# Performance work log

Hardware: AMD Instinct MI355X
Metric: run time of the kernel (lower is better)

The kernel has to match this reference:

```python
import jax, jax.numpy as jnp
import numpy as np

NHEAD = 8

def layernorm(x, g, b, eps=1e-5):
    mu = x.mean(-1, keepdims=True)
    var = ((x - mu) ** 2).mean(-1, keepdims=True)
    return (x - mu) / jnp.sqrt(var + eps) * g + b

def linear_attention(q, k, v, eps=1e-6):
    # LoFTR kernelized linear attention: phi(x) = elu(x) + 1
    Q = jax.nn.elu(q) + 1.0          # [n, l, h, d]
    K = jax.nn.elu(k) + 1.0          # [n, s, h, d]
    s_len = v.shape[1]
    KV = jnp.einsum("nshd,nshv->nhdv", K, v / s_len)
    Z = 1.0 / (jnp.einsum("nlhd,nhd->nlh", Q, K.sum(axis=1)) + eps)
    return jnp.einsum("nlhd,nhdv,nlh->nlhv", Q, KV, Z) * s_len

def _block(x_base, q, k, v, Wm, W1, W2, g1, b1, g2, b2):
    bs, L, h, dh = q.shape
    msg = linear_attention(q, k, v).reshape(bs, L, h * dh)
    msg = layernorm(msg @ Wm, g1, b1)
    hcat = jnp.concatenate([x_base, msg], axis=2)          # [bs, L, 2*d]
    out = jax.nn.relu(hcat @ W1) @ W2
    return layernorm(out, g2, b2)

def setup_inputs() -> dict:
    key = jax.random.key(0)
    ks = jax.random.split(key, 8)
    bs, L, S, d = 8, 4800, 4800, 256
    w = lambda k, i, o: jax.random.normal(k, (i, o), jnp.float32) * 0.02
    return {
        "x": jax.random.normal(ks[0], (bs, L, d), jnp.float32),
        "source": jax.random.normal(ks[1], (bs, S, d), jnp.float32),
        "Wq": w(ks[2], d, d), "Wk": w(ks[3], d, d), "Wv": w(ks[4], d, d),
        "Wm": w(ks[5], d, d),
        "W1": w(ks[6], 2 * d, 2 * d), "W2": w(ks[7], 2 * d, d),
        "g1": jnp.ones((d,), jnp.float32), "b1": jnp.zeros((d,), jnp.float32),
        "g2": jnp.ones((d,), jnp.float32), "b2": jnp.zeros((d,), jnp.float32),
    }

def reference(x, source, Wq, Wk, Wv, Wm, W1, W2, g1, b1, g2, b2):
    bs, L, d = x.shape
    h = NHEAD
    dh = d // h
    q = (x @ Wq).reshape(bs, L, h, dh)
    k = (source @ Wk).reshape(bs, -1, h, dh)
    v = (source @ Wv).reshape(bs, -1, h, dh)
    # permute-then-view reinterpretations, exactly as in the torch code
    p13 = lambda t: t.transpose(0, 1, 3, 2).reshape(bs, -1, h, dh)  # permute(0,1,3,2)
    p21 = lambda t: t.transpose(0, 2, 1, 3).reshape(bs, -1, h, dh)  # permute(0,2,1,3)
    p32 = lambda t: t.transpose(0, 3, 2, 1).reshape(bs, -1, h, dh)  # permute(0,3,2,1)
    blk = lambda xb, qq, kk, vv: _block(xb, qq, kk, vv, Wm, W1, W2, g1, b1, g2, b2)
    m = blk(x, q, k, v)
    m3 = blk(x, p13(q), p13(k), p13(v))
    x_mid = x + 0.5 * (m + m3)
    m1 = blk(x_mid, p21(q), p21(k), p21(v))
    m2 = blk(x_mid, p32(q), p32(k), p32(v))
    return x_mid + 0.5 * (m1 + m2)
```

## Files before the change

### kernel.cpp

```cpp
#include <hip/hip_runtime.h>
#include <type_traits>
#include <cstdint>
#include <cstddef>

#define L_SEQ 4800
#define DMODEL 256
#define BS 8
#define MROWS (BS*L_SEQ)
#define PERBATCH (L_SEQ*DMODEL)
#define KVSET 67584

typedef __attribute__((ext_vector_type(8))) short bfrag8;
typedef __attribute__((ext_vector_type(4))) float floatx4;

__device__ __forceinline__ float bf2f(unsigned short u){
  union { unsigned int i; float f; } x; x.i = ((unsigned int)u) << 16; return x.f;
}
__device__ __forceinline__ unsigned short f2bf(float f){
  union { float f; unsigned int i; } x; x.f = f;
  x.i += 0x7fff + ((x.i >> 16) & 1);
  return (unsigned short)(x.i >> 16);
}
__device__ __forceinline__ float phi(float x){
  return x > 0.f ? x + 1.f : __expf(x);
}
__device__ __forceinline__ void gll16(const void* g, void* l){
  __builtin_amdgcn_global_load_lds((const __attribute__((address_space(1))) unsigned int*)g,
      (__attribute__((address_space(3))) unsigned int*)l, 16, 0, 0);
}

template<typename TC, bool RELU>
__global__ __launch_bounds__(256) void gemm_mfma(const unsigned short* __restrict__ A,
                                                 const unsigned short* __restrict__ Bt,
                                                 TC* __restrict__ C, int M, int N, int K){
  __shared__ unsigned short Al[2][4096];
  __shared__ unsigned short Bl[2][4096];
  const int tid  = threadIdx.x;
  const int lane = tid & 63;
  const int wave = tid >> 6;
  const int row0 = blockIdx.y << 7;
  const int col0 = blockIdx.x << 7;
  const int wr0  = (wave & 1) << 6;
  const int wc0  = (wave >> 1) << 6;
  const int m = lane & 15, q = lane >> 4;
  const int sw = (m >> 1) & 3;

  floatx4 acc[4][4] = {};

  const int u0 = tid, u1 = tid + 256;
  const int r0 = u0 >> 2, s0 = u0 & 3;
  const int r1 = u1 >> 2, s1 = u1 & 3;

  auto stage = [&](int k0, int b){
    gll16(A  + (size_t)(row0 + r0)*K + k0 + ((s0 ^ ((r0 >> 1) & 3)) << 3), Al[b] + (size_t)u0*8);
    gll16(A  + (size_t)(row0 + r1)*K + k0 + ((s1 ^ ((r1 >> 1) & 3)) << 3), Al[b] + (size_t)u1*8);
    gll16(Bt + (size_t)(col0 + r0)*K + k0 + ((s0 ^ ((r0 >> 1) & 3)) << 3), Bl[b] + (size_t)u0*8);
    gll16(Bt + (size_t)(col0 + r1)*K + k0 + ((s1 ^ ((r1 >> 1) & 3)) << 3), Bl[b] + (size_t)u1*8);
  };

  stage(0, 0);
  const int nk = K >> 5;
  for (int ks = 0; ks < nk; ks++){
    asm volatile("s_waitcnt vmcnt(0) lgkmcnt(0)" ::: "memory");
    __builtin_amdgcn_s_barrier();
    asm volatile("" ::: "memory");
    if (ks < nk - 1) stage((ks + 1) << 5, (ks + 1) & 1);
    const unsigned short* ab = Al[ks & 1];
    const unsigned short* bb = Bl[ks & 1];
    bfrag8 af[4], bf[4];
    #pragma unroll
    for (int t = 0; t < 4; t++){
      af[t] = *(const bfrag8*)(ab + (size_t)(wr0 + t*16 + m)*32 + ((q ^ sw) << 3));
      bf[t] = *(const bfrag8*)(bb + (size_t)(wc0 + t*16 + m)*32 + ((q ^ sw) << 3));
    }
    #pragma unroll
    for (int mt = 0; mt < 4; mt++)
      #pragma unroll
      for (int nt = 0; nt < 4; nt++)
        acc[mt][nt] = __builtin_amdgcn_mfma_f32_16x16x32_bf16(af[mt], bf[nt], acc[mt][nt], 0, 0, 0);
  }

  #pragma unroll
  for (int mt = 0; mt < 4; mt++){
    #pragma unroll
    for (int nt = 0; nt < 4; nt++){
      const int col  = col0 + wc0 + nt*16 + m;
      const int rowb = row0 + wr0 + mt*16 + q*4;
      #pragma unroll
      for (int i = 0; i < 4; i++){
        float v = acc[mt][nt][i];
        if (RELU) v = v > 0.f ? v : 0.f;
        if constexpr (std::is_same<TC,float>::value) C[(size_t)(rowb+i)*N + col] = v;
        else                                         C[(size_t)(rowb+i)*N + col] = f2bf(v);
      }
    }
  }
}

__global__ __launch_bounds__(256) void wconv(const float* __restrict__ W, unsigned short* __restrict__ Wt,
                                             int kshift, int N){
  int idx = blockIdx.x*256 + threadIdx.x;
  int kk = idx & ((1 << kshift) - 1);
  int nn = idx >> kshift;
  Wt[idx] = f2bf(W[(size_t)kk*N + nn]);
}
__global__ __launch_bounds__(256) void conv_bf16(const float* __restrict__ in, unsigned short* __restrict__ out){
  int i = blockIdx.x*256 + threadIdx.x;
  float4 v = ((const float4*)in)[i];
  ushort4 o; o.x = f2bf(v.x); o.y = f2bf(v.y); o.z = f2bf(v.z); o.w = f2bf(v.w);
  ((ushort4*)out)[i] = o;
}

__global__ __launch_bounds__(256) void permute1(const unsigned short* __restrict__ sA, unsigned short* __restrict__ dA,
                                                const unsigned short* __restrict__ sB, unsigned short* __restrict__ dB){
  const unsigned short* s = blockIdx.z ? sB : sA;
  unsigned short*       d = blockIdx.z ? dB : dA;
  __shared__ unsigned short tile[1024];
  const int t = threadIdx.x;
  const size_t base = (size_t)blockIdx.x * 1024;
  #pragma unroll
  for (int i = 0; i < 4; i++) tile[i*256 + t] = s[base + i*256 + t];
  __syncthreads();
  const int pg = ((t & 7) << 5) + (t >> 3);
  #pragma unroll
  for (int i = 0; i < 4; i++) d[base + i*256 + t] = tile[i*256 + pg];
}

__global__ __launch_bounds__(256) void permute2(const unsigned short* __restrict__ sA, unsigned short* __restrict__ dA,
                                                const unsigned short* __restrict__ sB, unsigned short* __restrict__ dB){
  const unsigned short* s = blockIdx.z ? sB : sA;
  unsigned short*       d = blockIdx.z ? dB : dA;
  __shared__ unsigned short tile[64*256];
  const int t = threadIdx.x;
  const int rr0 = blockIdx.x * 64;
  const size_t boff = (size_t)blockIdx.y * PERBATCH;
  #pragma unroll
  for (int i = 0; i < 16; i++){
    int u = i*256 + t;
    *(ushort4*)&tile[u*4] = *(const ushort4*)&s[boff + (size_t)rr0*256 + (size_t)u*4];
  }
  __syncthreads();
  #pragma unroll
  for (int i = 0; i < 8; i++){
    #pragma unroll
    for (int w = 0; w < 2; w++){
      int u = w*256 + t;
      int rr = u >> 3, c4 = (u & 7) << 2;
      ushort4 v = *(const ushort4*)&tile[rr*256 + i*32 + c4];
      *(ushort4*)&d[boff + (size_t)i*153600 + (size_t)rr0*32 + (size_t)u*4] = v;
    }
  }
}

__global__ __launch_bounds__(256) void permute3(const unsigned short* __restrict__ sA, unsigned short* __restrict__ dA,
                                                const unsigned short* __restrict__ sB, unsigned short* __restrict__ dB){
  const unsigned short* s = blockIdx.z ? sB : sA;
  unsigned short*       d = blockIdx.z ? dB : dA;
  __shared__ unsigned short tile[64*258];
  const int t = threadIdx.x;
  const int ll0 = blockIdx.x * 64;
  const size_t boff = (size_t)blockIdx.y * PERBATCH;
  #pragma unroll
  for (int i = 0; i < 32; i++){
    int u = i*256 + t;
    int row = u >> 7, col = (u & 127) << 1;
    *(ushort2*)&tile[row*258 + col] = *(const ushort2*)&s[boff + (size_t)(ll0+row)*256 + col];
  }
  __syncthreads();
  const int cw = t >> 6;
  const int ll = t & 63;
  #pragma unroll
  for (int cc = 0; cc < 256; cc += 4){
    int c = cc + cw;
    int sigma = ((c & 31) << 3) + (c >> 5);
    d[boff + (size_t)sigma*4800 + ll0 + ll] = tile[ll*258 + c];
  }
}

__global__ __launch_bounds__(256) void attn_stats(const unsigned short* __restrict__ kq,
                                                  const unsigned short* __restrict__ vq,
                                                  float* __restrict__ KV, float* __restrict__ Ksum){
  const int chunk = blockIdx.x, h = blockIdx.y, n = blockIdx.z;
  const int t = threadIdx.x;
  const int d = t >> 3;
  const int w4 = (t & 7) << 2;
  const size_t boff = (size_t)n * PERBATCH;
  __shared__ float kb[8][32], vb[8][32];
  const int lr = t >> 5, lj = t & 31;
  float a0=0.f, a1=0.f, a2=0.f, a3=0.f, ks=0.f;
  const int s0 = chunk * 240;
  for (int s = s0; s < s0 + 240; s += 8){
    int srci = (s + lr)*256 + (h << 5) + lj;
    kb[lr][lj] = phi(bf2f(kq[boff + srci]));
    vb[lr][lj] = bf2f(vq[boff + srci]);
    __syncthreads();
    #pragma unroll
    for (int r = 0; r < 8; r++){
      float kd = kb[r][d];
      ks += kd;
      a0 += kd * vb[r][w4+0];
      a1 += kd * vb[r][w4+1];
      a2 += kd * vb[r][w4+2];
      a3 += kd * vb[r][w4+3];
    }
    __syncthreads();
  }
  float* kvp = KV + (size_t)((((n<<3)+h)<<5) + d)*32 + w4;
  atomicAdd(kvp+0, a0);
  atomicAdd(kvp+1, a1);
  atomicAdd(kvp+2, a2);
  atomicAdd(kvp+3, a3);
  if ((t & 7) == 0) atomicAdd(Ksum + (((n<<3)+h)<<5) + d, ks);
}

__global__ __launch_bounds__(256) void attn_fused(const unsigned short* __restrict__ qq,
                                                  const float* __restrict__ KV,
                                                  const float* __restrict__ Ksum,
                                                  const unsigned short* __restrict__ WmT,
                                                  const float* __restrict__ g1,
                                                  const float* __restrict__ b1,
                                                  unsigned short* __restrict__ hcat){
  __shared__ float kvs[8192];
  __shared__ float Qs[4096];
  __shared__ float kss[256];
  __shared__ char  msgL[8192];
  __shared__ float2 LNp[16][4];
  const int t = threadIdx.x;
  const int n = blockIdx.y;
  const int row0 = blockIdx.x << 4;
  const size_t boff = (size_t)n * PERBATCH;

  {
    const float4* kvsrc = (const float4*)(KV + (size_t)n*8192);
    #pragma unroll
    for (int i = 0; i < 8; i++) ((float4*)kvs)[i*256 + t] = kvsrc[i*256 + t];
    kss[t] = Ksum[n*256 + t];
    #pragma unroll
    for (int i = 0; i < 4; i++){
      int u = (i << 8) + t;
      int r = u >> 6, c4 = (u & 63) << 2;
      ushort4 v = *(const ushort4*)(qq + boff + (size_t)(row0 + r)*256 + c4);
      float4 f;
      f.x = phi(bf2f(v.x)); f.y = phi(bf2f(v.y)); f.z = phi(bf2f(v.z)); f.w = phi(bf2f(v.w));
      *(float4*)&Qs[r*256 + c4] = f;
    }
  }
  __syncthreads();

  {
    const int h = t >> 5, w = t & 31;
    const float* kvh = kvs + h*1024;
    const float* ksh = kss + h*32;
    float acc[16], den[16];
    #pragma unroll
    for (int r = 0; r < 16; r++){ acc[r] = 0.f; den[r] = 1e-6f; }
    #pragma unroll
    for (int d4 = 0; d4 < 8; d4++){
      const float k0 = kvh[(d4*4+0)*32 + w];
      const float k1 = kvh[(d4*4+1)*32 + w];
      const float k2 = kvh[(d4*4+2)*32 + w];
      const float k3 = kvh[(d4*4+3)*32 + w];
      const float s0 = ksh[d4*4+0], s1 = ksh[d4*4+1], s2 = ksh[d4*4+2], s3 = ksh[d4*4+3];
      #pragma unroll
      for (int r = 0; r < 16; r++){
        float4 qv = *(const float4*)&Qs[r*256 + h*32 + d4*4];
        acc[r] += qv.x*k0 + qv.y*k1 + qv.z*k2 + qv.w*k3;
        den[r] += qv.x*s0 + qv.y*s1 + qv.z*s2 + qv.w*s3;
      }
    }
    #pragma unroll
    for (int r = 0; r < 16; r++){
      int byte = (r << 9) + ((t << 1) ^ ((r & 7) << 4));
      *(unsigned short*)(msgL + byte) = f2bf(acc[r] / den[r]);
    }
  }
  __syncthreads();

  const int wv = t >> 6, lane = t & 63, m = lane & 15, qd = lane >> 4;
  floatx4 Cf[4] = {};
  #pragma unroll
  for (int ks = 0; ks < 8; ks++){
    int abyte = m*512 + ((ks*64 + qd*16) ^ ((m & 7) << 4));
    bfrag8 af = *(const bfrag8*)(msgL + abyte);
    #pragma unroll
    for (int nt = 0; nt < 4; nt++){
      int col = wv*64 + nt*16 + m;
      bfrag8 bf = *(const bfrag8*)(WmT + (size_t)col*256 + ks*32 + qd*8);
      Cf[nt] = __builtin_amdgcn_mfma_f32_16x16x32_bf16(af, bf, Cf[nt], 0, 0, 0);
    }
  }

  #pragma unroll
  for (int i = 0; i < 4; i++){
    float s = 0.f, q = 0.f;
    #pragma unroll
    for (int nt = 0; nt < 4; nt++){ float v = Cf[nt][i]; s += v; q += v*v; }
    #pragma unroll
    for (int o = 1; o < 16; o <<= 1){ s += __shfl_xor(s, o, 64); q += __shfl_xor(q, o, 64); }
    if (m == 0) LNp[qd*4 + i][wv] = make_float2(s, q);
  }
  __syncthreads();
  float gv[4], bv[4];
  #pragma unroll
  for (int nt = 0; nt < 4; nt++){ int col = wv*64 + nt*16 + m; gv[nt] = g1[col]; bv[nt] = b1[col]; }
  #pragma unroll
  for (int i = 0; i < 4; i++){
    int row = qd*4 + i;
    float2 p0 = LNp[row][0], p1 = LNp[row][1], p2 = LNp[row][2], p3 = LNp[row][3];
    float S = p0.x + p1.x + p2.x + p3.x;
    float Q = p0.y + p1.y + p2.y + p3.y;
    float mu = S * (1.f/256.f);
    float rs = rsqrtf(Q * (1.f/256.f) - mu*mu + 1e-5f);
    #pragma unroll
    for (int nt = 0; nt < 4; nt++){
      int col = wv*64 + nt*16 + m;
      *(unsigned short*)(msgL + row*512 + col*2) = f2bf((Cf[nt][i] - mu) * rs * gv[nt] + bv[nt]);
    }
  }
  __syncthreads();
  const size_t gbase = ((size_t)n*4800 + row0)*512 + 256;
  #pragma unroll
  for (int i = 0; i < 4; i++){
    int u = (i << 8) + t;
    int r = u >> 6, c4 = (u & 63) << 2;
    *(ushort4*)(hcat + gbase + (size_t)r*512 + c4) = *(const ushort4*)(msgL + r*512 + c4*2);
  }
}

__global__ __launch_bounds__(512) void ffn_fused(const unsigned short* __restrict__ hcat,
                                                 const unsigned short* __restrict__ W1T,
                                                 const unsigned short* __restrict__ W2T,
                                                 const float* __restrict__ g2,
                                                 const float* __restrict__ b2,
                                                 float* __restrict__ macc, int add){
  __shared__ char stg[139264];
  char* const hcdb = stg;
  char* const wdb  = stg + 8192;
  char* const hidL = stg + 8192 + 65536;
  const int tid = threadIdx.x;
  const int wv = tid >> 6, lane = tid & 63;
  const int m = lane & 15, qd = lane >> 4;
  const int sw = (m >> 1) & 3;
  const int row0 = blockIdx.x << 6;

  auto stage1 = [&](int ks, int b){
    const int k0 = ks << 5;
    if (tid < 256){
      int r = tid >> 2, s = tid & 3;
      gll16(hcat + (size_t)(row0 + r)*512 + k0 + ((s ^ ((r >> 1) & 3)) << 3),
            hcdb + (b << 12) + (tid << 4));
    }
    #pragma unroll
    for (int i = 0; i < 4; i++){
      int u = (i << 9) + tid;
      int c = u >> 2, s = u & 3;
      gll16(W1T + (size_t)c*512 + k0 + ((s ^ ((c >> 1) & 3)) << 3),
            wdb + (b << 15) + (u << 4));
    }
  };

  floatx4 acc1[4][4] = {};
  stage1(0, 0);
  for (int ks = 0; ks < 16; ks++){
    asm volatile("s_waitcnt vmcnt(0) lgkmcnt(0)" ::: "memory");
    __builtin_amdgcn_s_barrier();
    asm volatile("" ::: "memory");
    if (ks < 15) stage1(ks + 1, (ks + 1) & 1);
    const char* hb = hcdb + ((ks & 1) << 12);
    const char* wb = wdb + ((ks & 1) << 15);
    bfrag8 af[4], bf[4];
    #pragma unroll
    for (int t = 0; t < 4; t++){
      af[t] = *(const bfrag8*)(hb + (t*16 + m)*64 + ((qd ^ sw) << 4));
      bf[t] = *(const bfrag8*)(wb + (wv*64 + t*16 + m)*64 + ((qd ^ sw) << 4));
    }
    #pragma unroll
    for (int mt = 0; mt < 4; mt++)
      #pragma unroll
      for (int nt = 0; nt < 4; nt++)
        acc1[mt][nt] = __builtin_amdgcn_mfma_f32_16x16x32_bf16(af[mt], bf[nt], acc1[mt][nt], 0, 0, 0);
  }

  #pragma unroll
  for (int nt = 0; nt < 4; nt++){
    const int c  = wv*2 + (nt >> 1);
    const int kl = ((nt & 1) << 4) + m;
    const int slot = kl >> 3;
    #pragma unroll
    for (int mt = 0; mt < 4; mt++)
      #pragma unroll
      for (int i = 0; i < 4; i++){
        int row = mt*16 + qd*4 + i;
        float v = acc1[mt][nt][i];
        v = v > 0.f ? v : 0.f;
        int byte = (c << 12) + row*64 + ((slot ^ ((row >> 1) & 3)) << 4) + ((kl & 7) << 1);
        *(unsigned short*)(hidL + byte) = f2bf(v);
      }
  }

  auto stage2 = [&](int o, int b){
    const int k0 = o << 6;
    #pragma unroll
    for (int i = 0; i < 4; i++){
      int u = (i << 9) + tid;
      int c = u >> 3, s = u & 7;
      gll16(W2T + (size_t)c*512 + k0 + ((s ^ ((c >> 1) & 7)) << 3),
            wdb + (b << 15) + (u << 4));
    }
  };
  stage2(0, 0);

  floatx4 acc2[4][2] = {};
  for (int o = 0; o < 8; o++){
    asm volatile("s_waitcnt vmcnt(0) lgkmcnt(0)" ::: "memory");
    __builtin_amdgcn_s_barrier();
    asm volatile("" ::: "memory");
    if (o < 7) stage2(o + 1, (o + 1) & 1);
    const char* wb = wdb + ((o & 1) << 15);
    #pragma unroll
    for (int j = 0; j < 2; j++){
      const int ck = o*2 + j;
      bfrag8 af[4], bf[2];
      #pragma unroll
      for (int t = 0; t < 4; t++)
        af[t] = *(const bfrag8*)(hidL + (ck << 12) + (t*16 + m)*64 + ((qd ^ sw) << 4));
      #pragma unroll
      for (int nt = 0; nt < 2; nt++){
        int col = wv*32 + nt*16 + m;
        bf[nt] = *(const bfrag8*)(wb + col*128 + (((j*4 + qd) ^ ((col >> 1) & 7)) << 4));
      }
      #pragma unroll
      for (int mt = 0; mt < 4; mt++)
        #pragma unroll
        for (int nt = 0; nt < 2; nt++)
          acc2[mt][nt] = __builtin_amdgcn_mfma_f32_16x16x32_bf16(af[mt], bf[nt], acc2[mt][nt], 0, 0, 0);
    }
  }

  float2* LNp  = (float2*)stg;
  float2* LNmu = (float2*)(stg + 4096);
  #pragma unroll
  for (int mt = 0; mt < 4; mt++)
    #pragma unroll
    for (int i = 0; i < 4; i++){
      float s = 0.f, q = 0.f;
      #pragma unroll
      for (int nt = 0; nt < 2; nt++){ float v = acc2[mt][nt][i]; s += v; q += v*v; }
      #pragma unroll
      for (int o = 1; o < 16; o <<= 1){ s += __shfl_xor(s, o, 64); q += __shfl_xor(q, o, 64); }
      if (m == 0) LNp[(mt*16 + qd*4 + i)*8 + wv] = make_float2(s, q);
    }
  asm volatile("s_waitcnt lgkmcnt(0)" ::: "memory");
  __builtin_amdgcn_s_barrier();
  asm volatile("" ::: "memory");
  if (tid < 64){
    float S = 0.f, Q = 0.f;
    #pragma unroll
    for (int j = 0; j < 8; j++){ float2 p = LNp[tid*8 + j]; S += p.x; Q += p.y; }
    float mean = S * (1.f/256.f);
    float var  = Q * (1.f/256.f) - mean*mean;
    LNmu[tid] = make_float2(mean, rsqrtf(var + 1e-5f));
  }
  asm volatile("s_waitcnt lgkmcnt(0)" ::: "memory");
  __builtin_amdgcn_s_barrier();
  asm volatile("" ::: "memory");
  float gv[2], bv[2];
  #pragma unroll
  for (int nt = 0; nt < 2; nt++){ int col = wv*32 + nt*16 + m; gv[nt] = g2[col]; bv[nt] = b2[col]; }
  #pragma unroll
  for (int mt = 0; mt < 4; mt++)
    #pragma unroll
    for (int i = 0; i < 4; i++){
      int row = mt*16 + qd*4 + i;
      float2 ms = LNmu[row];
      #pragma unroll
      for (int nt = 0; nt < 2; nt++){
        float y = (acc2[mt][nt][i] - ms.x) * ms.y * gv[nt] + bv[nt];
        float* p = macc + (size_t)(row0 + row)*256 + wv*32 + nt*16 + m;
        if (add) y += *p;
        *p = y;
      }
    }
}

__global__ __launch_bounds__(256) void fill_hcat(const float* __restrict__ x, unsigned short* __restrict__ hcat){
  size_t i = (size_t)blockIdx.x*256 + threadIdx.x;
  hcat[(i >> 8)*512 + (i & 255)] = f2bf(x[i]);
}
__global__ __launch_bounds__(256) void xmid_k(const float* __restrict__ x, const float* __restrict__ macc,
                                              float* __restrict__ xmid, unsigned short* __restrict__ hcat){
  size_t i = (size_t)blockIdx.x*256 + threadIdx.x;
  float v = x[i] + 0.5f*macc[i];
  xmid[i] = v;
  hcat[(i >> 8)*512 + (i & 255)] = f2bf(v);
}
__global__ __launch_bounds__(256) void final_k(float* __restrict__ out, const float* __restrict__ macc){
  size_t i = (size_t)blockIdx.x*256 + threadIdx.x;
  out[i] = out[i] + 0.5f*macc[i];
}
__global__ __launch_bounds__(256) void zero_k(float* __restrict__ p, int n){
  int i = blockIdx.x*256 + threadIdx.x;
  if (i < n) p[i] = 0.f;
}

extern "C" void kernel_launch(void* const* d_in, const int* in_sizes, int n_in,
                              void* d_out, int out_size, void* d_ws, size_t ws_size,
                              hipStream_t stream){
  const float* x   = (const float*)d_in[0];
  const float* src = (const float*)d_in[1];
  const float* Wq  = (const float*)d_in[2];
  const float* Wk  = (const float*)d_in[3];
  const float* Wv  = (const float*)d_in[4];
  const float* Wm  = (const float*)d_in[5];
  const float* W1  = (const float*)d_in[6];
  const float* W2  = (const float*)d_in[7];
  const float* g1  = (const float*)d_in[8];
  const float* b1  = (const float*)d_in[9];
  const float* g2  = (const float*)d_in[10];
  const float* b2  = (const float*)d_in[11];
  float* out = (float*)d_out;

  char* ws = (char*)d_ws;
  size_t off = 0;
  auto alloc = [&](size_t bytes) -> void* {
    void* p = ws + off;
    off += (bytes + 255) & ~(size_t)255;
    return p;
  };
  unsigned short* qB    = (unsigned short*)alloc((size_t)MROWS*256*2);
  unsigned short* kB    = (unsigned short*)alloc((size_t)MROWS*256*2);
  unsigned short* vB    = (unsigned short*)alloc((size_t)MROWS*256*2);
  unsigned short* hcatB = (unsigned short*)alloc((size_t)MROWS*512*2);
  float* t1   = (float*)alloc((size_t)MROWS*256*4);
  float* macc = (float*)alloc((size_t)MROWS*256*4);
  float* KV4  = (float*)alloc((size_t)4*KVSET*4);
  unsigned short* WqT = (unsigned short*)alloc((size_t)256*256*2);
  unsigned short* WkT = (unsigned short*)alloc((size_t)256*256*2);
  unsigned short* WvT = (unsigned short*)alloc((size_t)256*256*2);
  unsigned short* WmT = (unsigned short*)alloc((size_t)256*256*2);
  unsigned short* W1T = (unsigned short*)alloc((size_t)512*512*2);
  unsigned short* W2T = (unsigned short*)alloc((size_t)256*512*2);
  (void)ws_size; (void)in_sizes; (void)n_in; (void)out_size;

  unsigned short* srcbf = (unsigned short*)t1;
  unsigned short* xbf   = srcbf + (size_t)MROWS*256;
  unsigned short* qP    = (unsigned short*)t1;
  unsigned short* kP    = (unsigned short*)macc;
  unsigned short* vP    = kP + (size_t)MROWS*256;
  float* xmid = out;

  const dim3 blk(256);

  wconv<<<dim3(256),  blk, 0, stream>>>(Wq, WqT, 8, 256);
  wconv<<<dim3(256),  blk, 0, stream>>>(Wk, WkT, 8, 256);
  wconv<<<dim3(256),  blk, 0, stream>>>(Wv, WvT, 8, 256);
  wconv<<<dim3(256),  blk, 0, stream>>>(Wm, WmT, 8, 256);
  wconv<<<dim3(1024), blk, 0, stream>>>(W1, W1T, 9, 512);
  wconv<<<dim3(512),  blk, 0, stream>>>(W2, W2T, 9, 256);
  conv_bf16<<<dim3(9600), blk, 0, stream>>>(src, srcbf);
  conv_bf16<<<dim3(9600), blk, 0, stream>>>(x,   xbf);

  gemm_mfma<unsigned short, false><<<dim3(2,300), blk, 0, stream>>>(xbf,   WqT, qB, MROWS, 256, 256);
  gemm_mfma<unsigned short, false><<<dim3(2,300), blk, 0, stream>>>(srcbf, WkT, kB, MROWS, 256, 256);
  gemm_mfma<unsigned short, false><<<dim3(2,300), blk, 0, stream>>>(srcbf, WvT, vB, MROWS, 256, 256);

  zero_k<<<dim3(1056), blk, 0, stream>>>(KV4, 4*KVSET);
  attn_stats<<<dim3(20,8,8), blk, 0, stream>>>(kB, vB, KV4 + 0*KVSET, KV4 + 0*KVSET + 65536);
  permute1<<<dim3(9600,1,2), blk, 0, stream>>>(kB, kP, vB, vP);
  attn_stats<<<dim3(20,8,8), blk, 0, stream>>>(kP, vP, KV4 + 1*KVSET, KV4 + 1*KVSET + 65536);
  permute2<<<dim3(75,8,2),  blk, 0, stream>>>(kB, kP, vB, vP);
  attn_stats<<<dim3(20,8,8), blk, 0, stream>>>(kP, vP, KV4 + 2*KVSET, KV4 + 2*KVSET + 65536);
  permute3<<<dim3(75,8,2),  blk, 0, stream>>>(kB, kP, vB, vP);
  attn_stats<<<dim3(20,8,8), blk, 0, stream>>>(kP, vP, KV4 + 3*KVSET, KV4 + 3*KVSET + 65536);

  fill_hcat<<<dim3(MROWS), blk, 0, stream>>>(x, hcatB);

  auto run_block = [&](int mode, int add){
    const float* KV   = KV4 + (size_t)mode*KVSET;
    const float* Ksum = KV + 65536;
    const unsigned short* qsrc = qB;
    if (mode == 1){ permute1<<<dim3(9600,1,1), blk, 0, stream>>>(qB, qP, nullptr, nullptr); qsrc = qP; }
    else if (mode == 2){ permute2<<<dim3(75,8,1), blk, 0, stream>>>(qB, qP, nullptr, nullptr); qsrc = qP; }
    else if (mode == 3){ permute3<<<dim3(75,8,1), blk, 0, stream>>>(qB, qP, nullptr, nullptr); qsrc = qP; }
    attn_fused<<<dim3(300,BS), blk, 0, stream>>>(qsrc, KV, Ksum, WmT, g1, b1, hcatB);
    ffn_fused<<<dim3(600), dim3(512), 0, stream>>>(hcatB, W1T, W2T, g2, b2, macc, add);
  };

  run_block(0, 0);
  run_block(1, 1);
  xmid_k<<<dim3(MROWS), blk, 0, stream>>>(x, macc, xmid, hcatB);
  run_block(2, 0);
  run_block(3, 1);
  final_k<<<dim3(MROWS), blk, 0, stream>>>(out, macc);
}
```

Before: 1.065 ms.

## Load FFN GEMM operands directly from global memory instead of LDS staging

The fused FFN kernel no longer double-buffers hcat and W1/W2 tiles into shared memory with async global-to-LDS copies and per-step barriers. Each wave now reads its MFMA fragments straight from global memory (relying on L2/L1 caching of the weights), and only the hidden activation stays in LDS. Shared memory drops from about 136 KB to about 70 KB and launch bounds request more blocks per CU, aiming for higher occupancy and fewer barriers. The risk is uncoalesced 16-byte fragment loads and redundant weight traffic, since the eight waves and all blocks re-read the weights through the cache.

```diff
diff --git a/kernel.cpp b/kernel.cpp
--- a/kernel.cpp
+++ b/kernel.cpp
@@ -327,52 +327,31 @@
   }
 }
 
-__global__ __launch_bounds__(512) void ffn_fused(const unsigned short* __restrict__ hcat,
-                                                 const unsigned short* __restrict__ W1T,
-                                                 const unsigned short* __restrict__ W2T,
-                                                 const float* __restrict__ g2,
-                                                 const float* __restrict__ b2,
-                                                 float* __restrict__ macc, int add){
-  __shared__ char stg[139264];
-  char* const hcdb = stg;
-  char* const wdb  = stg + 8192;
-  char* const hidL = stg + 8192 + 65536;
+__global__ __launch_bounds__(512, 4) void ffn_fused(const unsigned short* __restrict__ hcat,
+                                                    const unsigned short* __restrict__ W1T,
+                                                    const unsigned short* __restrict__ W2T,
+                                                    const float* __restrict__ g2,
+                                                    const float* __restrict__ b2,
+                                                    float* __restrict__ macc, int add){
+  __shared__ char hidL[65536];
+  __shared__ float2 LNp[64*8];
+  __shared__ float2 LNmu[64];
   const int tid = threadIdx.x;
   const int wv = tid >> 6, lane = tid & 63;
   const int m = lane & 15, qd = lane >> 4;
   const int sw = (m >> 1) & 3;
   const int row0 = blockIdx.x << 6;
 
-  auto stage1 = [&](int ks, int b){
-    const int k0 = ks << 5;
-    if (tid < 256){
-      int r = tid >> 2, s = tid & 3;
-      gll16(hcat + (size_t)(row0 + r)*512 + k0 + ((s ^ ((r >> 1) & 3)) << 3),
-            hcdb + (b << 12) + (tid << 4));
-    }
-    #pragma unroll
-    for (int i = 0; i < 4; i++){
-      int u = (i << 9) + tid;
-      int c = u >> 2, s = u & 3;
-      gll16(W1T + (size_t)c*512 + k0 + ((s ^ ((c >> 1) & 3)) << 3),
-            wdb + (b << 15) + (u << 4));
-    }
-  };
-
+  const unsigned short* Abase = hcat + (size_t)row0*512 + qd*8;
+  const unsigned short* Bbase = W1T + (size_t)(wv*64 + m)*512 + qd*8;
   floatx4 acc1[4][4] = {};
-  stage1(0, 0);
+  #pragma unroll
   for (int ks = 0; ks < 16; ks++){
-    asm volatile("s_waitcnt vmcnt(0) lgkmcnt(0)" ::: "memory");
-    __builtin_amdgcn_s_barrier();
-    asm volatile("" ::: "memory");
-    if (ks < 15) stage1(ks + 1, (ks + 1) & 1);
-    const char* hb = hcdb + ((ks & 1) << 12);
-    const char* wb = wdb + ((ks & 1) << 15);
     bfrag8 af[4], bf[4];
     #pragma unroll
     for (int t = 0; t < 4; t++){
-      af[t] = *(const bfrag8*)(hb + (t*16 + m)*64 + ((qd ^ sw) << 4));
-      bf[t] = *(const bfrag8*)(wb + (wv*64 + t*16 + m)*64 + ((qd ^ sw) << 4));
+      af[t] = *(const bfrag8*)(Abase + (size_t)(t*16 + m)*512 + ks*32);
+      bf[t] = *(const bfrag8*)(Bbase + (size_t)(t*16)*512 + ks*32);
     }
     #pragma unroll
     for (int mt = 0; mt < 4; mt++)
@@ -397,48 +376,26 @@
         *(unsigned short*)(hidL + byte) = f2bf(v);
       }
   }
-
-  auto stage2 = [&](int o, int b){
-    const int k0 = o << 6;
-    #pragma unroll
-    for (int i = 0; i < 4; i++){
-      int u = (i << 9) + tid;
-      int c = u >> 3, s = u & 7;
-      gll16(W2T + (size_t)c*512 + k0 + ((s ^ ((c >> 1) & 7)) << 3),
-            wdb + (b << 15) + (u << 4));
-    }
-  };
-  stage2(0, 0);
-
+  __syncthreads();
+
+  const unsigned short* B2base = W2T + (size_t)(wv*32 + m)*512 + qd*8;
   floatx4 acc2[4][2] = {};
-  for (int o = 0; o < 8; o++){
-    asm volatile("s_waitcnt vmcnt(0) lgkmcnt(0)" ::: "memory");
-    __builtin_amdgcn_s_barrier();
-    asm volatile("" ::: "memory");
-    if (o < 7) stage2(o + 1, (o + 1) & 1);
-    const char* wb = wdb + ((o & 1) << 15);
-    #pragma unroll
-    for (int j = 0; j < 2; j++){
-      const int ck = o*2 + j;
-      bfrag8 af[4], bf[2];
-      #pragma unroll
-      for (int t = 0; t < 4; t++)
-        af[t] = *(const bfrag8*)(hidL + (ck << 12) + (t*16 + m)*64 + ((qd ^ sw) << 4));
-      #pragma unroll
-      for (int nt = 0; nt < 2; nt++){
-        int col = wv*32 + nt*16 + m;
-        bf[nt] = *(const bfrag8*)(wb + col*128 + (((j*4 + qd) ^ ((col >> 1) & 7)) << 4));
-      }
-      #pragma unroll
-      for (int mt = 0; mt < 4; mt++)
-        #pragma unroll
-        for (int nt = 0; nt < 2; nt++)
-          acc2[mt][nt] = __builtin_amdgcn_mfma_f32_16x16x32_bf16(af[mt], bf[nt], acc2[mt][nt], 0, 0, 0);
-    }
-  }
-
-  float2* LNp  = (float2*)stg;
-  float2* LNmu = (float2*)(stg + 4096);
+  #pragma unroll
+  for (int ks = 0; ks < 16; ks++){
+    bfrag8 af[4], bf[2];
+    #pragma unroll
+    for (int t = 0; t < 4; t++)
+      af[t] = *(const bfrag8*)(hidL + (ks << 12) + (t*16 + m)*64 + ((qd ^ sw) << 4));
+    #pragma unroll
+    for (int nt = 0; nt < 2; nt++)
+      bf[nt] = *(const bfrag8*)(B2base + (size_t)(nt*16)*512 + ks*32);
+    #pragma unroll
+    for (int mt = 0; mt < 4; mt++)
+      #pragma unroll
+      for (int nt = 0; nt < 2; nt++)
+        acc2[mt][nt] = __builtin_amdgcn_mfma_f32_16x16x32_bf16(af[mt], bf[nt], acc2[mt][nt], 0, 0, 0);
+  }
+
   #pragma unroll
   for (int mt = 0; mt < 4; mt++)
     #pragma unroll
@@ -450,9 +407,7 @@
       for (int o = 1; o < 16; o <<= 1){ s += __shfl_xor(s, o, 64); q += __shfl_xor(q, o, 64); }
       if (m == 0) LNp[(mt*16 + qd*4 + i)*8 + wv] = make_float2(s, q);
     }
-  asm volatile("s_waitcnt lgkmcnt(0)" ::: "memory");
-  __builtin_amdgcn_s_barrier();
-  asm volatile("" ::: "memory");
+  __syncthreads();
   if (tid < 64){
     float S = 0.f, Q = 0.f;
     #pragma unroll
@@ -461,9 +416,7 @@
     float var  = Q * (1.f/256.f) - mean*mean;
     LNmu[tid] = make_float2(mean, rsqrtf(var + 1e-5f));
   }
-  asm volatile("s_waitcnt lgkmcnt(0)" ::: "memory");
-  __builtin_amdgcn_s_barrier();
-  asm volatile("" ::: "memory");
+  __syncthreads();
   float gv[2], bv[2];
   #pragma unroll
   for (int nt = 0; nt < 2; nt++){ int col = wv*32 + nt*16 + m; gv[nt] = g2[col]; bv[nt] = b2[col]; }
```

Measured after the change: 1.258 ms. +18.1%, slower.
